# Optimization experiments

Measured on AMD Instinct MI355X. Metric: run time of the kernel, lower is better.

Reference implementation:

```python
import jax, jax.numpy as jnp
import numpy as np

# Dims
B, S, D = 4, 4096, 1024
H, NB, A = 4, 4096, 4          # hashes, buckets, associativity
DK, DV, DT = 64, 128, 32        # key dim, value (mem) dim, vsa tag dim
BITS = 12                       # log2(NB)
TEMP = 1.0
VSA_W = 1.0
TANH_SCALE = 1.0
ETA = 0.1
WRITE_THR = 0.5
MATCH_THR = 0.0
NOV_THR = 0.0
EPS = 1e-6


def _l2n(x):
    return x / (jnp.linalg.norm(x, axis=-1, keepdims=True) + EPS)


def setup_inputs() -> dict:
    key = jax.random.key(0)
    ks = jax.random.split(key, 13)
    sc = 0.02
    return {
        "u": jax.random.normal(ks[0], (B, S, D), jnp.float32),
        "memK": jax.random.normal(ks[1], (H, NB, A, DK), jnp.float32),
        "memV": jax.random.normal(ks[2], (H, NB, A, DV), jnp.float32),
        "memT": jnp.tanh(jax.random.normal(ks[3], (H, NB, A, DT), jnp.float32)),
        "Wq": jax.random.normal(ks[4], (DK, D), jnp.float32) * sc,
        "Wwk": jax.random.normal(ks[5], (DK, D), jnp.float32) * sc,
        "Wv": jax.random.normal(ks[6], (DV, D), jnp.float32) * sc,
        "Wo": jax.random.normal(ks[7], (D, DV), jnp.float32) * sc,
        "Wg": jax.random.normal(ks[8], (1, D), jnp.float32) * sc,
        "bg": jnp.zeros((1,), jnp.float32),
        "Wvsa": jax.random.normal(ks[9], (DK, DT), jnp.float32) * sc,
        "R": jax.random.normal(ks[10], (H, DK, BITS), jnp.float32),
    }


def reference(u, memK, memV, memT, Wq, Wwk, Wv, Wo, Wg, bg, Wvsa, R):
    N = B * S
    uf = u.reshape(N, D)

    # ---- routing: sign-bit LSH over query key -> bucket index per hash ----
    qkey = uf @ Wq.T                                     # [N, DK]
    bits = (jnp.einsum("nd,hdk->nhk", qkey, R) > 0).astype(jnp.int32)
    pw = (2 ** jnp.arange(BITS, dtype=jnp.int32))
    idx = (bits * pw).sum(-1)                            # [N, H] bucket ids
    hh = jnp.arange(H)[None, :]                          # [1, H]

    # ---- associative gather read ----
    Kg = memK[hh, idx]                                   # [N, H, A, DK]
    Vg = memV[hh, idx]                                   # [N, H, A, DV]
    Tg = memT[hh, idx]                                   # [N, H, A, DT]
    qtag = jnp.tanh(TANH_SCALE * (qkey @ Wvsa))          # [N, DT]
    sc = (jnp.einsum("nd,nhad->nha", qkey, Kg) / np.sqrt(DK)
          + VSA_W * jnp.einsum("nt,nhat->nha", qtag, Tg) / np.sqrt(DT))
    w = jax.nn.softmax(sc.reshape(N, H * A) / TEMP, axis=-1)
    read = jnp.einsum("nk,nkd->nd", w, Vg.reshape(N, H * A, DV))
    y = (read @ Wo.T).reshape(B, S, D)

    # ---- gated scatter write with EMA + novelty ----
    wkey = uf @ Wwk.T                                    # [N, DK]
    wval = uf @ Wv.T                                     # [N, DV]
    gate = jax.nn.sigmoid(uf @ Wg.T + bg)                # [N, 1]
    wmask = (gate > WRITE_THR).astype(u.dtype)           # [N, 1]
    wtag = jnp.tanh(TANH_SCALE * (wkey @ Wvsa))          # [N, DT]

    sim = jnp.einsum("nd,nhad->nha", _l2n(wkey), _l2n(Kg))   # [N,H,A]
    astar = jnp.argmax(sim, axis=-1)                         # [N,H]
    bsim = jnp.max(sim, axis=-1)                             # [N,H]
    take = lambda G: jnp.take_along_axis(G, astar[:, :, None, None], axis=2)[:, :, 0]
    Kbest, Vbest, Tbest = take(Kg), take(Vg), take(Tg)       # [N,H,·]

    tagsim = jnp.einsum("nt,nhat->nha", _l2n(wtag), _l2n(Tg))
    novelty = 1.0 - jnp.max(tagsim, axis=-1)                 # [N,H]

    eff = (ETA * gate * wmask
           * (bsim >= MATCH_THR).astype(u.dtype)
           * (novelty >= NOV_THR).astype(u.dtype))           # [N,H]

    dK = eff[..., None] * (wkey[:, None, :] - Kbest)
    dV = eff[..., None] * (wval[:, None, :] - Vbest)
    dT = eff[..., None] * (wtag[:, None, :] - Tbest)
    Knew = memK.at[hh, idx, astar].add(dK)
    Vnew = memV.at[hh, idx, astar].add(dV)
    Tnew = memT.at[hh, idx, astar].add(dT)
    return y, Knew, Vnew, Tnew
```

## Files before the change

### kernel.cpp

```cpp
#include <hip/hip_runtime.h>
#include <hip/hip_bf16.h>
#include <math.h>

#define NTOK    16384
#define DMODEL  1024
#define HN      4
#define NBUCKET 4096
#define ASSOC   4
#define DKEY    64
#define DVAL    128
#define DTAG    32
#define NBITS   12
#define EPSV    1e-6f

typedef __bf16 bf16x8 __attribute__((ext_vector_type(8)));
typedef float  f32x4  __attribute__((ext_vector_type(4)));
typedef float  f32x2  __attribute__((ext_vector_type(2)));

__device__ __forceinline__ unsigned short f2bf_raw(float f) {
    __hip_bfloat16 h = __float2bfloat16(f);
    return *(unsigned short*)&h;
}

__global__ __launch_bounds__(256) void gemm_mfma(const float* __restrict__ A,
                                                 const float* __restrict__ B,
                                                 float* __restrict__ C,
                                                 int M, int N, int K) {
    __shared__ __align__(16) unsigned short As[4][128][8];
    __shared__ __align__(16) unsigned short Bs[4][128][8];
    const int t    = threadIdx.x;
    const int lane = t & 63;
    const int w    = t >> 6;
    const int wm   = (w & 1) * 64;
    const int wn   = (w >> 1) * 64;
    const int bm   = blockIdx.x * 128;
    const int bn   = blockIdx.y * 128;

    const int srow = t & 127;
    const int skg  = t >> 7;
    const float* Ap = A + (size_t)(bm + srow) * K;
    const float* Bp = B + (size_t)(bn + srow) * K;

    const int fr = lane & 15;
    const int kq = lane >> 4;

    f32x4 acc[4][4] = {};

    for (int k0 = 0; k0 < K; k0 += 32) {
        #pragma unroll
        for (int ii = 0; ii < 2; ++ii) {
            const int kg = skg + ii * 2;
            const float4 a0 = *(const float4*)(Ap + k0 + kg * 8);
            const float4 a1 = *(const float4*)(Ap + k0 + kg * 8 + 4);
            const float4 b0 = *(const float4*)(Bp + k0 + kg * 8);
            const float4 b1 = *(const float4*)(Bp + k0 + kg * 8 + 4);
            unsigned short* da = &As[kg][srow][0];
            da[0] = f2bf_raw(a0.x); da[1] = f2bf_raw(a0.y);
            da[2] = f2bf_raw(a0.z); da[3] = f2bf_raw(a0.w);
            da[4] = f2bf_raw(a1.x); da[5] = f2bf_raw(a1.y);
            da[6] = f2bf_raw(a1.z); da[7] = f2bf_raw(a1.w);
            unsigned short* db = &Bs[kg][srow][0];
            db[0] = f2bf_raw(b0.x); db[1] = f2bf_raw(b0.y);
            db[2] = f2bf_raw(b0.z); db[3] = f2bf_raw(b0.w);
            db[4] = f2bf_raw(b1.x); db[5] = f2bf_raw(b1.y);
            db[6] = f2bf_raw(b1.z); db[7] = f2bf_raw(b1.w);
        }
        __syncthreads();
        bf16x8 af[4], bfv[4];
        #pragma unroll
        for (int i = 0; i < 4; ++i) af[i]  = *(const bf16x8*)&As[kq][wm + i * 16 + fr][0];
        #pragma unroll
        for (int j = 0; j < 4; ++j) bfv[j] = *(const bf16x8*)&Bs[kq][wn + j * 16 + fr][0];
        #pragma unroll
        for (int i = 0; i < 4; ++i)
            #pragma unroll
            for (int j = 0; j < 4; ++j)
                acc[i][j] = __builtin_amdgcn_mfma_f32_16x16x32_bf16(af[i], bfv[j], acc[i][j], 0, 0, 0);
        __syncthreads();
    }
    #pragma unroll
    for (int i = 0; i < 4; ++i)
        #pragma unroll
        for (int j = 0; j < 4; ++j)
            #pragma unroll
            for (int r = 0; r < 4; ++r)
                C[(size_t)(bm + wm + i * 16 + kq * 4 + r) * N + (bn + wn + j * 16 + fr)] = acc[i][j][r];
}

__global__ __launch_bounds__(256) void gemm_wval_splitk(const float* __restrict__ A,
                                                        const float* __restrict__ B,
                                                        float* __restrict__ Cpart) {
    __shared__ __align__(16) unsigned short As[4][128][8];
    __shared__ __align__(16) unsigned short Bs[4][128][8];
    const int t    = threadIdx.x;
    const int lane = t & 63;
    const int w    = t >> 6;
    const int wm   = (w & 1) * 64;
    const int wn   = (w >> 1) * 64;
    const int bm   = blockIdx.x * 128;
    const int kz   = blockIdx.y;
    const int kbeg = kz * 256;

    const int srow = t & 127;
    const int skg  = t >> 7;
    const float* Ap = A + (size_t)(bm + srow) * DMODEL;
    const float* Bp = B + (size_t)srow * DMODEL;

    const int fr = lane & 15;
    const int kq = lane >> 4;

    f32x4 acc[4][4] = {};

    for (int k0 = kbeg; k0 < kbeg + 256; k0 += 32) {
        #pragma unroll
        for (int ii = 0; ii < 2; ++ii) {
            const int kg = skg + ii * 2;
            const float4 a0 = *(const float4*)(Ap + k0 + kg * 8);
            const float4 a1 = *(const float4*)(Ap + k0 + kg * 8 + 4);
            const float4 b0 = *(const float4*)(Bp + k0 + kg * 8);
            const float4 b1 = *(const float4*)(Bp + k0 + kg * 8 + 4);
            unsigned short* da = &As[kg][srow][0];
            da[0] = f2bf_raw(a0.x); da[1] = f2bf_raw(a0.y);
            da[2] = f2bf_raw(a0.z); da[3] = f2bf_raw(a0.w);
            da[4] = f2bf_raw(a1.x); da[5] = f2bf_raw(a1.y);
            da[6] = f2bf_raw(a1.z); da[7] = f2bf_raw(a1.w);
            unsigned short* db = &Bs[kg][srow][0];
            db[0] = f2bf_raw(b0.x); db[1] = f2bf_raw(b0.y);
            db[2] = f2bf_raw(b0.z); db[3] = f2bf_raw(b0.w);
            db[4] = f2bf_raw(b1.x); db[5] = f2bf_raw(b1.y);
            db[6] = f2bf_raw(b1.z); db[7] = f2bf_raw(b1.w);
        }
        __syncthreads();
        bf16x8 af[4], bfv[4];
        #pragma unroll
        for (int i = 0; i < 4; ++i) af[i]  = *(const bf16x8*)&As[kq][wm + i * 16 + fr][0];
        #pragma unroll
        for (int j = 0; j < 4; ++j) bfv[j] = *(const bf16x8*)&Bs[kq][wn + j * 16 + fr][0];
        #pragma unroll
        for (int i = 0; i < 4; ++i)
            #pragma unroll
            for (int j = 0; j < 4; ++j)
                acc[i][j] = __builtin_amdgcn_mfma_f32_16x16x32_bf16(af[i], bfv[j], acc[i][j], 0, 0, 0);
        __syncthreads();
    }
    float* Cp = Cpart + (size_t)kz * NTOK * 128;
    #pragma unroll
    for (int i = 0; i < 4; ++i)
        #pragma unroll
        for (int j = 0; j < 4; ++j)
            #pragma unroll
            for (int r = 0; r < 4; ++r)
                Cp[(size_t)(bm + wm + i * 16 + kq * 4 + r) * 128 + (wn + j * 16 + fr)] = acc[i][j][r];
}

__global__ __launch_bounds__(256) void gemm_f32_splitk(const float* __restrict__ A,
                                                       const float* __restrict__ B,
                                                       float* __restrict__ Cpart,
                                                       int M, int K, int K_quarter) {
    __shared__ __align__(16) float As[2][16][68];
    __shared__ __align__(16) float Bs[2][16][140];
    const int t  = threadIdx.x;
    const int bm = blockIdx.x * 64;
    const int kz = blockIdx.z;
    const int tx = t & 15;
    const int ty = t >> 4;

    const int arow = t >> 2, ac = (t & 3) * 4;
    const int brow = t >> 1, bc = (t & 1) * 8;
    const int bperm = brow + ((brow >> 5) << 2);
    const int goff  = tx * 8 + ((tx >> 2) << 2);

    const float* Apt = A + (size_t)(bm + arow) * K + ac;
    const float* Bpt = B + (size_t)brow * K + bc;

    const int kbeg = kz * K_quarter;
    const int NSTEP = 16;

    f32x2 acc2[4][4] = {};

    float4 av = *(const float4*)(Apt + kbeg);
    float4 b0 = *(const float4*)(Bpt + kbeg);
    float4 b1 = *(const float4*)(Bpt + kbeg + 4);
    As[0][ac + 0][arow] = av.x; As[0][ac + 1][arow] = av.y;
    As[0][ac + 2][arow] = av.z; As[0][ac + 3][arow] = av.w;
    Bs[0][bc + 0][bperm] = b0.x; Bs[0][bc + 1][bperm] = b0.y;
    Bs[0][bc + 2][bperm] = b0.z; Bs[0][bc + 3][bperm] = b0.w;
    Bs[0][bc + 4][bperm] = b1.x; Bs[0][bc + 5][bperm] = b1.y;
    Bs[0][bc + 6][bperm] = b1.z; Bs[0][bc + 7][bperm] = b1.w;
    __syncthreads();

    for (int s = 0; s < NSTEP; ++s) {
        const int cur = s & 1;
        if (s + 1 < NSTEP) {
            const int k0 = kbeg + (s + 1) * 16;
            av = *(const float4*)(Apt + k0);
            b0 = *(const float4*)(Bpt + k0);
            b1 = *(const float4*)(Bpt + k0 + 4);
        }
        #pragma unroll
        for (int kk = 0; kk < 16; ++kk) {
            const float4 a4 = *(const float4*)&As[cur][kk][ty * 4];
            const float4 v0 = *(const float4*)&Bs[cur][kk][goff];
            const float4 v1 = *(const float4*)&Bs[cur][kk][goff + 4];
            const float aa[4] = {a4.x, a4.y, a4.z, a4.w};
            const f32x2 bb[4] = {{v0.x, v0.y}, {v0.z, v0.w}, {v1.x, v1.y}, {v1.z, v1.w}};
            #pragma unroll
            for (int i = 0; i < 4; ++i) {
                const f32x2 as2 = {aa[i], aa[i]};
                #pragma unroll
                for (int j = 0; j < 4; ++j)
                    acc2[i][j] = __builtin_elementwise_fma(as2, bb[j], acc2[i][j]);
            }
        }
        if (s + 1 < NSTEP) {
            const int nb = cur ^ 1;
            As[nb][ac + 0][arow] = av.x; As[nb][ac + 1][arow] = av.y;
            As[nb][ac + 2][arow] = av.z; As[nb][ac + 3][arow] = av.w;
            Bs[nb][bc + 0][bperm] = b0.x; Bs[nb][bc + 1][bperm] = b0.y;
            Bs[nb][bc + 2][bperm] = b0.z; Bs[nb][bc + 3][bperm] = b0.w;
            Bs[nb][bc + 4][bperm] = b1.x; Bs[nb][bc + 5][bperm] = b1.y;
            Bs[nb][bc + 6][bperm] = b1.z; Bs[nb][bc + 7][bperm] = b1.w;
        }
        __syncthreads();
    }

    float* Cp = Cpart + (size_t)kz * M * 128;
    #pragma unroll
    for (int i = 0; i < 4; ++i) {
        float4 o0, o1;
        o0.x = acc2[i][0].x; o0.y = acc2[i][0].y; o0.z = acc2[i][1].x; o0.w = acc2[i][1].y;
        o1.x = acc2[i][2].x; o1.y = acc2[i][2].y; o1.z = acc2[i][3].x; o1.w = acc2[i][3].y;
        float* dst = &Cp[(size_t)(bm + ty * 4 + i) * 128 + tx * 8];
        *(float4*)dst       = o0;
        *(float4*)(dst + 4) = o1;
    }
}

__global__ __launch_bounds__(256) void route_kernel(
    const float* __restrict__ memK, const float* __restrict__ memV,
    const float* __restrict__ memT, const float* __restrict__ R,
    const float* __restrict__ Wvsa,
    const float* __restrict__ partQ, const float* __restrict__ partW,
    const float* __restrict__ u, const float* __restrict__ Wg,
    const float* __restrict__ bg,
    float* __restrict__ accK, float* __restrict__ accV, float* __restrict__ accT,
    float* __restrict__ readw) {
    __shared__ float sQK[4][64], sWK[4][64], sQT[4][32], sWT[4][32];
    __shared__ float sSc[4][16], sSim[4][16], sTsim[4][16], sW[4][16];
    __shared__ int   sIdx[4][4], sAst[4][4];
    __shared__ float sEff[4][4];

    const int wv = threadIdx.x >> 6;
    const int lane = threadIdx.x & 63;
    const int n = blockIdx.x * 4 + wv;
    const size_t PZ = (size_t)NTOK * 128;

    const size_t qb = (size_t)n * 128;
    const float qk = (partQ[qb + lane]          + partQ[PZ + qb + lane])
                   + (partQ[2 * PZ + qb + lane] + partQ[3 * PZ + qb + lane]);
    const float wk = (partQ[qb + 64 + lane]          + partQ[PZ + qb + 64 + lane])
                   + (partQ[2 * PZ + qb + 64 + lane] + partQ[3 * PZ + qb + 64 + lane]);
    sQK[wv][lane] = qk;
    sWK[wv][lane] = wk;
    float wk2 = wk * wk;
    #pragma unroll
    for (int off = 1; off < 64; off <<= 1) wk2 += __shfl_xor(wk2, off);
    const float wknorm = sqrtf(wk2) + EPSV;

    float gacc = 0.f;
    {
        const float* up = u + (size_t)n * DMODEL;
        #pragma unroll
        for (int j = 0; j < 16; ++j)
            gacc += up[lane + 64 * j] * Wg[lane + 64 * j];
        #pragma unroll
        for (int off = 1; off < 64; off <<= 1) gacc += __shfl_xor(gacc, off);
    }
    const float gate = 1.f / (1.f + expf(-(gacc + bg[0])));
    __syncthreads();

    {
        const int tg = lane & 31;
        const float* keyp = (lane < 32) ? sQK[wv] : sWK[wv];
        float tacc = 0.f;
        for (int d = 0; d < 64; ++d) tacc += keyp[d] * Wvsa[d * DTAG + tg];
        const float tagv = tanhf(tacc);
        if (lane < 32) sQT[wv][tg] = tagv; else sWT[wv][tg] = tagv;
        float wt2 = (lane >= 32) ? tagv * tagv : 0.f;
        #pragma unroll
        for (int off = 1; off < 64; off <<= 1) wt2 += __shfl_xor(wt2, off);
        const float wtnorm = sqrtf(wt2) + EPSV;

        bool bit = false;
        if (lane < 48) {
            const int h = lane / 12, k = lane % 12;
            float bacc = 0.f;
            for (int d = 0; d < 64; ++d)
                bacc += sQK[wv][d] * R[(size_t)(h * DKEY + d) * NBITS + k];
            bit = bacc > 0.f;
        }
        const unsigned long long mask = __ballot(bit);
        if (lane < 4) sIdx[wv][lane] = (int)((mask >> (12 * lane)) & 0xFFFull);
        __syncthreads();

        const int slot = lane >> 2, sub = lane & 3;
        const int sh = slot >> 2, sa = slot & 3;
        const int rowS = (sh * NBUCKET + sIdx[wv][sh]) * ASSOC + sa;
        const float* Kp = memK + (size_t)rowS * DKEY;
        const float* Tp = memT + (size_t)rowS * DTAG;
        float d_qk = 0, d_wk = 0, d_kk = 0, d_qt = 0, d_wt = 0, d_tt = 0;
        for (int j = 0; j < 16; ++j) {
            const int d = sub * 16 + j;
            const float kv = Kp[d];
            d_qk += sQK[wv][d] * kv;
            d_wk += sWK[wv][d] * kv;
            d_kk += kv * kv;
        }
        for (int j = 0; j < 8; ++j) {
            const int d = sub * 8 + j;
            const float tv = Tp[d];
            d_qt += sQT[wv][d] * tv;
            d_wt += sWT[wv][d] * tv;
            d_tt += tv * tv;
        }
        #pragma unroll
        for (int off = 1; off <= 2; off <<= 1) {
            d_qk += __shfl_xor(d_qk, off);
            d_wk += __shfl_xor(d_wk, off);
            d_kk += __shfl_xor(d_kk, off);
            d_qt += __shfl_xor(d_qt, off);
            d_wt += __shfl_xor(d_wt, off);
            d_tt += __shfl_xor(d_tt, off);
        }
        if (sub == 0) {
            sSc[wv][slot]   = d_qk * 0.125f + d_qt * 0.17677669529663687f;
            sSim[wv][slot]  = d_wk / (wknorm * (sqrtf(d_kk) + EPSV));
            sTsim[wv][slot] = d_wt / (wtnorm * (sqrtf(d_tt) + EPSV));
        }
    }
    __syncthreads();

    if (lane < 16) {
        const float sc = sSc[wv][lane];
        float m = sc;
        #pragma unroll
        for (int off = 1; off < 16; off <<= 1) m = fmaxf(m, __shfl_xor(m, off, 16));
        const float e = expf(sc - m);
        float ssum = e;
        #pragma unroll
        for (int off = 1; off < 16; off <<= 1) ssum += __shfl_xor(ssum, off, 16);
        sW[wv][lane] = e / ssum;
    }
    if (lane < 4) {
        float bs = -1e30f; int as = 0; float mt = -1e30f;
        #pragma unroll
        for (int aa = 0; aa < 4; ++aa) {
            const float sv = sSim[wv][lane * 4 + aa];
            if (sv > bs) { bs = sv; as = aa; }
            mt = fmaxf(mt, sTsim[wv][lane * 4 + aa]);
        }
        const float novelty = 1.f - mt;
        float e = 0.1f * gate;
        if (!(gate > 0.5f) || !(bs >= 0.f) || !(novelty >= 0.f)) e = 0.f;
        sEff[wv][lane] = e;
        sAst[wv][lane] = as;
    }
    __syncthreads();

    float r0 = 0.f, r1 = 0.f;
    #pragma unroll
    for (int s2 = 0; s2 < 16; ++s2) {
        const int hh = s2 >> 2, aa = s2 & 3;
        const int rw = (hh * NBUCKET + sIdx[wv][hh]) * ASSOC + aa;
        const float wgt = sW[wv][s2];
        const float* Vp = memV + (size_t)rw * DVAL;
        r0 += wgt * Vp[lane];
        r1 += wgt * Vp[64 + lane];
    }
    readw[(size_t)n * DVAL + lane]      = r0;
    readw[(size_t)n * DVAL + 64 + lane] = r1;

    const float wv0 = (partW[qb + lane]          + partW[PZ + qb + lane])
                    + (partW[2 * PZ + qb + lane] + partW[3 * PZ + qb + lane]);
    const float wv1 = (partW[qb + 64 + lane]          + partW[PZ + qb + 64 + lane])
                    + (partW[2 * PZ + qb + 64 + lane] + partW[3 * PZ + qb + 64 + lane]);
    for (int hh = 0; hh < 4; ++hh) {
        const float e = sEff[wv][hh];
        if (e == 0.f) continue;
        const int rw = (hh * NBUCKET + sIdx[wv][hh]) * ASSOC + sAst[wv][hh];
        atomicAdd(&accK[(size_t)rw * DKEY + lane],
                  e * (sWK[wv][lane] - memK[(size_t)rw * DKEY + lane]));
        atomicAdd(&accV[(size_t)rw * DVAL + lane],
                  e * (wv0 - memV[(size_t)rw * DVAL + lane]));
        atomicAdd(&accV[(size_t)rw * DVAL + 64 + lane],
                  e * (wv1 - memV[(size_t)rw * DVAL + 64 + lane]));
        if (lane < 32)
            atomicAdd(&accT[(size_t)rw * DTAG + lane],
                      e * (sWT[wv][lane] - memT[(size_t)rw * DTAG + lane]));
    }
}

extern "C" void kernel_launch(void* const* d_in, const int* in_sizes, int n_in,
                              void* d_out, int out_size, void* d_ws, size_t ws_size,
                              hipStream_t stream) {
    const float* u    = (const float*)d_in[0];
    const float* memK = (const float*)d_in[1];
    const float* memV = (const float*)d_in[2];
    const float* memT = (const float*)d_in[3];
    const float* Wq   = (const float*)d_in[4];
    const float* Wwk  = (const float*)d_in[5];
    const float* Wv   = (const float*)d_in[6];
    const float* Wo   = (const float*)d_in[7];
    const float* Wg   = (const float*)d_in[8];
    const float* bg   = (const float*)d_in[9];
    const float* Wvsa = (const float*)d_in[10];
    const float* R    = (const float*)d_in[11];

    const int nK = HN * NBUCKET * ASSOC * DKEY;
    const int nV = HN * NBUCKET * ASSOC * DVAL;
    const int nT = HN * NBUCKET * ASSOC * DTAG;

    float* y_out = (float*)d_out;
    float* K_out = y_out + (size_t)NTOK * DMODEL;
    float* V_out = K_out + nK;
    float* T_out = V_out + nV;

    float* readw = (float*)d_ws;
    float* qwW   = readw + (size_t)NTOK * 128;

    float* partQ = y_out;
    float* partW = y_out + (size_t)4 * NTOK * 128;

    hipMemcpyAsync(qwW,          Wq,  (size_t)DKEY * DMODEL * 4, hipMemcpyDeviceToDevice, stream);
    hipMemcpyAsync(qwW + 65536,  Wwk, (size_t)DKEY * DMODEL * 4, hipMemcpyDeviceToDevice, stream);

    gemm_f32_splitk<<<dim3(NTOK / 64, 1, 4), 256, 0, stream>>>(u, qwW, partQ, NTOK, DMODEL, DMODEL / 4);

    gemm_wval_splitk<<<dim3(NTOK / 128, 4), 256, 0, stream>>>(u, Wv, partW);

    hipMemcpyAsync(K_out, memK, (size_t)nK * 4, hipMemcpyDeviceToDevice, stream);
    hipMemcpyAsync(V_out, memV, (size_t)nV * 4, hipMemcpyDeviceToDevice, stream);
    hipMemcpyAsync(T_out, memT, (size_t)nT * 4, hipMemcpyDeviceToDevice, stream);

    route_kernel<<<NTOK / 4, 256, 0, stream>>>(memK, memV, memT, R, Wvsa,
                                               partQ, partW, u, Wg, bg,
                                               K_out, V_out, T_out, readw);

    gemm_mfma<<<dim3(NTOK / 128, DMODEL / 128), 256, 0, stream>>>(readw, Wo, y_out, NTOK, DMODEL, DVAL);
}
```

Baseline: 401.3 us.

## Fuse gate dot product into split-K key GEMM to avoid rereading u

Computes the per-token gate logit partials inside the split-K Wq/Wwk GEMM, reusing the u tiles already staged in shared memory, and writes four partials per token to workspace. The routing kernel then sums these partials instead of reading a full row of u and Wg per token. This removes a second full pass over the large input activation. It adds a small amount of LDS reads and a workspace buffer to the GEMM.

```diff
diff --git a/kernel.cpp b/kernel.cpp
--- a/kernel.cpp
+++ b/kernel.cpp
@@ -155,10 +155,13 @@
 
 __global__ __launch_bounds__(256) void gemm_f32_splitk(const float* __restrict__ A,
                                                        const float* __restrict__ B,
+                                                       const float* __restrict__ Wg,
                                                        float* __restrict__ Cpart,
+                                                       float* __restrict__ gatep,
                                                        int M, int K, int K_quarter) {
     __shared__ __align__(16) float As[2][16][68];
     __shared__ __align__(16) float Bs[2][16][140];
+    __shared__ float sWg[256];
     const int t  = threadIdx.x;
     const int bm = blockIdx.x * 64;
     const int kz = blockIdx.z;
@@ -176,7 +179,10 @@
     const int kbeg = kz * K_quarter;
     const int NSTEP = 16;
 
+    if (t < 64) *(float4*)&sWg[t * 4] = *(const float4*)(Wg + kbeg + t * 4);
+
     f32x2 acc2[4][4] = {};
+    float gacc = 0.f;
 
     float4 av = *(const float4*)(Apt + kbeg);
     float4 b0 = *(const float4*)(Bpt + kbeg);
@@ -212,6 +218,13 @@
                     acc2[i][j] = __builtin_elementwise_fma(as2, bb[j], acc2[i][j]);
             }
         }
+        {
+            float ga = 0.f;
+            #pragma unroll
+            for (int kk = 0; kk < 4; ++kk)
+                ga += As[cur][ac + kk][arow] * sWg[s * 16 + ac + kk];
+            gacc += ga;
+        }
         if (s + 1 < NSTEP) {
             const int nb = cur ^ 1;
             As[nb][ac + 0][arow] = av.x; As[nb][ac + 1][arow] = av.y;
@@ -224,6 +237,13 @@
         __syncthreads();
     }
 
+    {
+        float g = gacc;
+        g += __shfl_xor(g, 1);
+        g += __shfl_xor(g, 2);
+        if ((t & 3) == 0) gatep[(size_t)kz * NTOK + bm + arow] = g;
+    }
+
     float* Cp = Cpart + (size_t)kz * M * 128;
     #pragma unroll
     for (int i = 0; i < 4; ++i) {
@@ -241,8 +261,7 @@
     const float* __restrict__ memT, const float* __restrict__ R,
     const float* __restrict__ Wvsa,
     const float* __restrict__ partQ, const float* __restrict__ partW,
-    const float* __restrict__ u, const float* __restrict__ Wg,
-    const float* __restrict__ bg,
+    const float* __restrict__ gatep, const float* __restrict__ bg,
     float* __restrict__ accK, float* __restrict__ accV, float* __restrict__ accT,
     float* __restrict__ readw) {
     __shared__ float sQK[4][64], sWK[4][64], sQT[4][32], sWT[4][32];
@@ -267,16 +286,10 @@
     for (int off = 1; off < 64; off <<= 1) wk2 += __shfl_xor(wk2, off);
     const float wknorm = sqrtf(wk2) + EPSV;
 
-    float gacc = 0.f;
-    {
-        const float* up = u + (size_t)n * DMODEL;
-        #pragma unroll
-        for (int j = 0; j < 16; ++j)
-            gacc += up[lane + 64 * j] * Wg[lane + 64 * j];
-        #pragma unroll
-        for (int off = 1; off < 64; off <<= 1) gacc += __shfl_xor(gacc, off);
-    }
-    const float gate = 1.f / (1.f + expf(-(gacc + bg[0])));
+    float gl = bg[0];
+    #pragma unroll
+    for (int z = 0; z < 4; ++z) gl += gatep[(size_t)z * NTOK + n];
+    const float gate = 1.f / (1.f + expf(-gl));
     __syncthreads();
 
     {
@@ -427,6 +440,7 @@
 
     float* readw = (float*)d_ws;
     float* qwW   = readw + (size_t)NTOK * 128;
+    float* gatep = qwW   + (size_t)128 * DMODEL;
 
     float* partQ = y_out;
     float* partW = y_out + (size_t)4 * NTOK * 128;
@@ -434,7 +448,8 @@
     hipMemcpyAsync(qwW,          Wq,  (size_t)DKEY * DMODEL * 4, hipMemcpyDeviceToDevice, stream);
     hipMemcpyAsync(qwW + 65536,  Wwk, (size_t)DKEY * DMODEL * 4, hipMemcpyDeviceToDevice, stream);
 
-    gemm_f32_splitk<<<dim3(NTOK / 64, 1, 4), 256, 0, stream>>>(u, qwW, partQ, NTOK, DMODEL, DMODEL / 4);
+    gemm_f32_splitk<<<dim3(NTOK / 64, 1, 4), 256, 0, stream>>>(u, qwW, Wg, partQ, gatep,
+                                                               NTOK, DMODEL, DMODEL / 4);
 
     gemm_wval_splitk<<<dim3(NTOK / 128, 4), 256, 0, stream>>>(u, Wv, partW);
 
@@ -443,7 +458,7 @@
     hipMemcpyAsync(T_out, memT, (size_t)nT * 4, hipMemcpyDeviceToDevice, stream);
 
     route_kernel<<<NTOK / 4, 256, 0, stream>>>(memK, memV, memT, R, Wvsa,
-                                               partQ, partW, u, Wg, bg,
+                                               partQ, partW, gatep, bg,
                                                K_out, V_out, T_out, readw);
 
     gemm_mfma<<<dim3(NTOK / 128, DMODEL / 128), 256, 0, stream>>>(readw, Wo, y_out, NTOK, DMODEL, DVAL);
```

After: 434.4 us. 8.3% more time.
